# Kernel optimization log

Hardware: AMD Instinct MI355X
Metric: run time of the kernel (lower is better)

## Reference

```python
import jax, jax.numpy as jnp
import numpy as np

N, R, B, H, C, E = 4096, 8, 30, 64, 16, 131072


def setup_inputs() -> dict:
    key = jax.random.key(0)
    ks = jax.random.split(key, 11)
    s = 0.02  # small init scale for weights
    return {
        "x": jax.random.normal(ks[0], (N, N), jnp.float32),
        "edge_index": jax.random.randint(ks[1], (2, E), 0, N, jnp.int32),
        "edge_type": jax.random.randint(ks[2], (E,), 0, R, jnp.int32),
        "basis1": jax.random.normal(ks[3], (B, N, H), jnp.float32) * s,
        "att1": jax.random.normal(ks[4], (R, B), jnp.float32) * s,
        "root1": jax.random.normal(ks[5], (N, H), jnp.float32) * s,
        "bias1": jnp.zeros((H,), jnp.float32),
        "basis2": jax.random.normal(ks[6], (B, H, C), jnp.float32) * s,
        "att2": jax.random.normal(ks[7], (R, B), jnp.float32) * s,
        "root2": jax.random.normal(ks[8], (H, C), jnp.float32) * s,
        "bias2": jnp.zeros((C,), jnp.float32),
    }


def _rgcn_conv(x, src, dst, etype, deg_inv, basis, att, root, bias):
    # Basis-decomposed relation weights: W_r = sum_b att[r,b] * basis[b]
    W = jnp.einsum("rb,bio->rio", att, basis)            # [R, in, out]
    # Pre-transform every node by every relation weight (equivalent to
    # per-edge bmm(x_j, W[edge_type]) but avoids gathering [E, in] features).
    h = jnp.einsum("ni,rio->nro", x, W)                  # [N, R, out]
    msg = h[src, etype]                                  # [E, out] per-edge message
    agg = jax.ops.segment_sum(msg, dst, num_segments=N)  # scatter-add to dst
    agg = agg * deg_inv[:, None]                         # scatter-mean (aggr='mean')
    return agg + x @ root + bias                         # root/self transform + bias


def reference(x, edge_index, edge_type, basis1, att1, root1, bias1,
              basis2, att2, root2, bias2):
    src, dst = edge_index[0], edge_index[1]
    deg = jax.ops.segment_sum(jnp.ones((E,), jnp.float32), dst, num_segments=N)
    deg_inv = 1.0 / jnp.maximum(deg, 1.0)  # zero in-degree -> 0 output, as scatter_mean
    h = jax.nn.relu(_rgcn_conv(x, src, dst, edge_type, deg_inv,
                               basis1, att1, root1, bias1))
    out = _rgcn_conv(h, src, dst, edge_type, deg_inv,
                     basis2, att2, root2, bias2)
    return jax.nn.log_softmax(out, axis=1)
```

## Files before the change

### kernel.cpp

```cpp
#include <hip/hip_runtime.h>
#include <cstdint>

#define E_CNT 131072
#define N_CNT 4096

typedef short bf16x8 __attribute__((ext_vector_type(8)));
typedef float f32x4 __attribute__((ext_vector_type(4)));

__device__ __forceinline__ ushort f2bf(float f) {
  union { float f; unsigned u; } v; v.f = f;
  unsigned r = v.u + 0x7FFFu + ((v.u >> 16) & 1u);
  return (ushort)(r >> 16);
}

__global__ __launch_bounds__(256) void k_prep(const float4* __restrict__ x,
                                              ushort* __restrict__ xbf,
                                              const int* __restrict__ dstp,
                                              int* __restrict__ deg,
                                              const float* __restrict__ att1,
                                              const float* __restrict__ basis1,
                                              const float* __restrict__ root1,
                                              ushort* __restrict__ wt1,
                                              int* __restrict__ c1i) {
  __shared__ float sT[32 * 33];
  int bid = blockIdx.x, t = threadIdx.x;
  if (bid < 16384) {
    int i = bid * 256 + t;
    float4 v = x[i];
    ushort4 o;
    o.x = f2bf(v.x); o.y = f2bf(v.y); o.z = f2bf(v.z); o.w = f2bf(v.w);
    *(ushort4*)(xbf + (size_t)i * 4) = o;
  } else if (bid < 16896) {
    int e = (bid - 16384) * 256 + t;
    atomicAdd(&deg[dstp[e]], 1);
  } else if (bid < 17152) {
    int bb = bid - 16896;
    int i0 = (bb >> 1) * 32, o0 = (bb & 1) * 32;
    int ol = t & 31, ir = t >> 5;
    float a[8][4] = {};
    for (int b = 0; b < 30; ++b) {
      float w0 = att1[0 * 30 + b], w1 = att1[1 * 30 + b], w2 = att1[2 * 30 + b], w3 = att1[3 * 30 + b];
      float w4 = att1[4 * 30 + b], w5 = att1[5 * 30 + b], w6 = att1[6 * 30 + b], w7 = att1[7 * 30 + b];
#pragma unroll
      for (int k = 0; k < 4; ++k) {
        float v = basis1[(size_t)b * 262144 + (size_t)(i0 + ir + k * 8) * 64 + o0 + ol];
        a[0][k] += w0 * v; a[1][k] += w1 * v; a[2][k] += w2 * v; a[3][k] += w3 * v;
        a[4][k] += w4 * v; a[5][k] += w5 * v; a[6][k] += w6 * v; a[7][k] += w7 * v;
      }
    }
    for (int r = 0; r < 8; ++r) {
#pragma unroll
      for (int k = 0; k < 4; ++k) sT[ol * 33 + ir + k * 8] = a[r][k];
      __syncthreads();
#pragma unroll
      for (int k = 0; k < 4; ++k) {
        int orow = ir + k * 8, icol = ol;
        wt1[(size_t)(r * 64 + o0 + orow) * 4096 + i0 + icol] = f2bf(sT[orow * 33 + icol]);
      }
      __syncthreads();
    }
  } else if (bid < 17168) {
    int bb = bid - 17152;
    int i0 = bb * 256;
    int ol = t & 31, ir = t >> 5;
    for (int s = 0; s < 8; ++s) {
      int ib = i0 + s * 32;
#pragma unroll
      for (int k = 0; k < 4; ++k) {
      }
      for (int oh = 0; oh < 2; ++oh) {
        int o0 = oh * 32;
#pragma unroll
        for (int k = 0; k < 4; ++k)
          sT[ol * 33 + ir + k * 8] = root1[(size_t)(ib + ir + k * 8) * 64 + o0 + ol];
        __syncthreads();
#pragma unroll
        for (int k = 0; k < 4; ++k) {
          int orow = ir + k * 8, icol = ol;
          wt1[(size_t)(512 + o0 + orow) * 4096 + ib + icol] = f2bf(sT[orow * 33 + icol]);
        }
        __syncthreads();
      }
    }
  } else {
    int flat = (bid - 17168) * 256 + t;
    c1i[flat] = 0;
  }
}

__global__ __launch_bounds__(1024) void k_scan(const int* __restrict__ deg,
                                               int* __restrict__ rowptr,
                                               int* __restrict__ cursor,
                                               float* __restrict__ dinv) {
  __shared__ int part[1024];
  int t = threadIdx.x;
  int base = t * 4;
  int d0 = deg[base], d1 = deg[base + 1], d2 = deg[base + 2], d3 = deg[base + 3];
  int s = d0 + d1 + d2 + d3;
  part[t] = s;
  __syncthreads();
  for (int off = 1; off < 1024; off <<= 1) {
    int v = part[t];
    int u = (t >= off) ? part[t - off] : 0;
    __syncthreads();
    part[t] = v + u;
    __syncthreads();
  }
  int incl = part[t];
  int excl = incl - s;
  int p0 = excl, p1 = excl + d0, p2 = p1 + d1, p3 = p2 + d2;
  rowptr[base] = p0; rowptr[base + 1] = p1; rowptr[base + 2] = p2; rowptr[base + 3] = p3;
  cursor[base] = p0; cursor[base + 1] = p1; cursor[base + 2] = p2; cursor[base + 3] = p3;
  dinv[base]     = 1.0f / fmaxf((float)d0, 1.0f);
  dinv[base + 1] = 1.0f / fmaxf((float)d1, 1.0f);
  dinv[base + 2] = 1.0f / fmaxf((float)d2, 1.0f);
  dinv[base + 3] = 1.0f / fmaxf((float)d3, 1.0f);
  if (t == 1023) rowptr[4096] = incl;
}

__global__ __launch_bounds__(256) void k_mid(const int* __restrict__ srcp,
                                             const int* __restrict__ dstp,
                                             const int* __restrict__ et,
                                             int* __restrict__ cursor,
                                             int* __restrict__ spack,
                                             const float* __restrict__ att2,
                                             const float* __restrict__ basis2,
                                             const float* __restrict__ root2,
                                             float* __restrict__ w2e) {
  int bid = blockIdx.x, t = threadIdx.x;
  if (bid < 512) {
    int e = bid * 256 + t;
    int d = dstp[e];
    int pos = atomicAdd(&cursor[d], 1);
    spack[pos] = (srcp[e] << 3) | et[e];
  } else {
    int r = bid - 512;
    for (int q = t; q < 1024; q += 256) {
      float a = 0.f;
      if (r < 8) {
        for (int b = 0; b < 30; ++b) a += att2[r * 30 + b] * basis2[b * 1024 + q];
      } else {
        a = root2[q];
      }
      w2e[r * 1024 + q] = a;
    }
  }
}

__global__ __launch_bounds__(256, 5) void k_gemm1(const ushort* __restrict__ xbf,
                                                  const ushort* __restrict__ wt1,
                                                  float* __restrict__ c1) {
  __shared__ __align__(16) ushort As[128 * 64];
  __shared__ __align__(16) ushort Bs[64 * 64];
  int bid = blockIdx.x;
  int swz = (bid & 7) * 144 + (bid >> 3);
  int kp = swz / 288, t2 = swz % 288;
  int bm = t2 / 9, bn = t2 % 9;
  int m0 = bm * 128, n0 = bn * 64, kbase = kp * 1024;
  int tid = threadIdx.x;
  int lane = tid & 63, wid = tid >> 6;
  int wm = wid >> 1, wn = wid & 1;

  f32x4 acc[4][2] = {};

  for (int tt = 0; tt < 16; ++tt) {
    int k0 = kbase + tt * 64;
#pragma unroll
    for (int it = 0; it < 4; ++it) {
      int flat = it * 256 + tid;
      int row = flat >> 3, gg = flat & 7;
      int gcol = k0 + ((gg ^ (row & 7)) << 3);
      const ushort* g = xbf + (size_t)(m0 + row) * 4096 + gcol;
      ushort* l = &As[(it * 256 + wid * 64) * 8];
      __builtin_amdgcn_global_load_lds((const __attribute__((address_space(1))) void*)g,
                                       (__attribute__((address_space(3))) void*)l, 16, 0, 0);
    }
#pragma unroll
    for (int it = 0; it < 2; ++it) {
      int flat = it * 256 + tid;
      int row = flat >> 3, gg = flat & 7;
      int gcol = k0 + ((gg ^ (row & 7)) << 3);
      const ushort* g = wt1 + (size_t)(n0 + row) * 4096 + gcol;
      ushort* l = &Bs[(it * 256 + wid * 64) * 8];
      __builtin_amdgcn_global_load_lds((const __attribute__((address_space(1))) void*)g,
                                       (__attribute__((address_space(3))) void*)l, 16, 0, 0);
    }
    __syncthreads();
    int q = lane >> 4, sw = lane & 7, r16 = lane & 15;
#pragma unroll
    for (int ks = 0; ks < 2; ++ks) {
      int co = ((ks * 4 + q) ^ sw) << 3;
      bf16x8 b0 = *(const bf16x8*)&Bs[(wn * 32 + 0 * 16 + r16) * 64 + co];
      bf16x8 b1 = *(const bf16x8*)&Bs[(wn * 32 + 1 * 16 + r16) * 64 + co];
      bf16x8 a0 = *(const bf16x8*)&As[(wm * 64 + 0 * 16 + r16) * 64 + co];
      bf16x8 a1 = *(const bf16x8*)&As[(wm * 64 + 1 * 16 + r16) * 64 + co];
      bf16x8 a2 = *(const bf16x8*)&As[(wm * 64 + 2 * 16 + r16) * 64 + co];
      bf16x8 a3 = *(const bf16x8*)&As[(wm * 64 + 3 * 16 + r16) * 64 + co];
      __builtin_amdgcn_s_setprio(1);
      acc[0][0] = __builtin_amdgcn_mfma_f32_16x16x32_bf16(a0, b0, acc[0][0], 0, 0, 0);
      acc[0][1] = __builtin_amdgcn_mfma_f32_16x16x32_bf16(a0, b1, acc[0][1], 0, 0, 0);
      acc[1][0] = __builtin_amdgcn_mfma_f32_16x16x32_bf16(a1, b0, acc[1][0], 0, 0, 0);
      acc[1][1] = __builtin_amdgcn_mfma_f32_16x16x32_bf16(a1, b1, acc[1][1], 0, 0, 0);
      acc[2][0] = __builtin_amdgcn_mfma_f32_16x16x32_bf16(a2, b0, acc[2][0], 0, 0, 0);
      acc[2][1] = __builtin_amdgcn_mfma_f32_16x16x32_bf16(a2, b1, acc[2][1], 0, 0, 0);
      acc[3][0] = __builtin_amdgcn_mfma_f32_16x16x32_bf16(a3, b0, acc[3][0], 0, 0, 0);
      acc[3][1] = __builtin_amdgcn_mfma_f32_16x16x32_bf16(a3, b1, acc[3][1], 0, 0, 0);
      __builtin_amdgcn_s_setprio(0);
    }
    __syncthreads();
  }

  int cf = lane & 15, rf4 = (lane >> 4) * 4;
#pragma unroll
  for (int mi = 0; mi < 4; ++mi)
#pragma unroll
    for (int ni = 0; ni < 2; ++ni) {
      int gcol = n0 + wn * 32 + ni * 16 + cf;
#pragma unroll
      for (int j = 0; j < 4; ++j) {
        int grow = m0 + wm * 64 + mi * 16 + rf4 + j;
        atomicAdd(&c1[(size_t)grow * 576 + gcol], acc[mi][ni][j]);
      }
    }
}

__global__ __launch_bounds__(256) void k_agg1h2(const float* __restrict__ c1,
                                                const int* __restrict__ rowptr,
                                                const int* __restrict__ spack,
                                                const float* __restrict__ dinv,
                                                const float* __restrict__ bias1,
                                                const float* __restrict__ w2e,
                                                float* __restrict__ h2c) {
  __shared__ float sh[4][64];
  int g = threadIdx.x >> 6, t = threadIdx.x & 63;
  int n = blockIdx.x * 4 + g;
  int s0 = rowptr[n], s1 = rowptr[n + 1];
  float acc = 0.f;
  int e = s0;
  for (; e + 3 < s1; e += 4) {
    int p0 = spack[e], p1 = spack[e + 1], p2 = spack[e + 2], p3 = spack[e + 3];
    float v0 = c1[(size_t)(p0 >> 3) * 576 + (p0 & 7) * 64 + t];
    float v1 = c1[(size_t)(p1 >> 3) * 576 + (p1 & 7) * 64 + t];
    float v2 = c1[(size_t)(p2 >> 3) * 576 + (p2 & 7) * 64 + t];
    float v3 = c1[(size_t)(p3 >> 3) * 576 + (p3 & 7) * 64 + t];
    acc += (v0 + v1) + (v2 + v3);
  }
  for (; e < s1; ++e) {
    int p = spack[e];
    acc += c1[(size_t)(p >> 3) * 576 + (p & 7) * 64 + t];
  }
  float v = acc * dinv[n] + c1[(size_t)n * 576 + 512 + t] + bias1[t];
  sh[g][t] = fmaxf(v, 0.f);
  __syncthreads();
  float* o = h2c + (size_t)n * 144;
  for (int rc = t; rc < 144; rc += 64) {
    int r9 = rc >> 4, c = rc & 15;
    const float* w = w2e + r9 * 1024 + c;
    float a = 0.f;
#pragma unroll
    for (int hh = 0; hh < 64; ++hh) a += sh[g][hh] * w[hh * 16];
    o[rc] = a;
  }
}

__global__ __launch_bounds__(64) void k_agg2(const float* __restrict__ h2c,
                                             const int* __restrict__ rowptr,
                                             const int* __restrict__ spack,
                                             const float* __restrict__ dinv,
                                             const float* __restrict__ bias2,
                                             float* __restrict__ out) {
  __shared__ float red[64];
  int n = blockIdx.x, t = threadIdx.x;
  int c = t & 15, q = t >> 4;
  int s0 = rowptr[n], s1 = rowptr[n + 1];
  float acc = 0.f;
  for (int e = s0 + q; e < s1; e += 4) {
    int p = spack[e];
    acc += h2c[(size_t)(p >> 3) * 144 + (p & 7) * 16 + c];
  }
  red[t] = acc;
  __syncthreads();
  if (t < 16) {
    float sum = red[c] + red[16 + c] + red[32 + c] + red[48 + c];
    float v = sum * dinv[n] + h2c[(size_t)n * 144 + 128 + c] + bias2[c];
    float m = v;
#pragma unroll
    for (int off = 1; off < 16; off <<= 1) m = fmaxf(m, __shfl_xor(m, off, 64));
    float ex = expf(v - m);
    float s = ex;
#pragma unroll
    for (int off = 1; off < 16; off <<= 1) s += __shfl_xor(s, off, 64);
    out[n * 16 + c] = v - m - logf(s);
  }
}

extern "C" void kernel_launch(void* const* d_in, const int* in_sizes, int n_in,
                              void* d_out, int out_size, void* d_ws, size_t ws_size,
                              hipStream_t stream) {
  const float* x      = (const float*)d_in[0];
  const int*   ei     = (const int*)d_in[1];
  const int*   et     = (const int*)d_in[2];
  const float* basis1 = (const float*)d_in[3];
  const float* att1   = (const float*)d_in[4];
  const float* root1  = (const float*)d_in[5];
  const float* bias1  = (const float*)d_in[6];
  const float* basis2 = (const float*)d_in[7];
  const float* att2   = (const float*)d_in[8];
  const float* root2  = (const float*)d_in[9];
  const float* bias2  = (const float*)d_in[10];
  float* out = (float*)d_out;

  char* ws = (char*)d_ws;
  size_t off = 0;
  auto alloc = [&](size_t bytes) {
    void* p = ws + off;
    off = (off + bytes + 255) & ~(size_t)255;
    return p;
  };
  ushort* xbf  = (ushort*)alloc((size_t)N_CNT * N_CNT * 2);
  ushort* wt1  = (ushort*)alloc((size_t)576 * 4096 * 2);
  float*  c1   = (float*)alloc((size_t)N_CNT * 576 * 4);
  float*  w2e  = (float*)alloc((size_t)9 * 64 * 16 * 4);
  float*  h2c  = (float*)alloc((size_t)N_CNT * 144 * 4);
  int*    deg    = (int*)alloc(4096 * 4);
  float*  dinv   = (float*)alloc(4096 * 4);
  int*    rowptr = (int*)alloc(4097 * 4);
  int*    cursor = (int*)alloc(4096 * 4);
  int*    spack  = (int*)alloc((size_t)E_CNT * 4);

  const int* srcp = ei;
  const int* dstp = ei + E_CNT;

  hipMemsetAsync(deg, 0, 4096 * 4, stream);
  k_prep<<<26384, 256, 0, stream>>>((const float4*)x, xbf, dstp, deg,
                                    att1, basis1, root1, wt1, (int*)c1);
  k_scan<<<1, 1024, 0, stream>>>(deg, rowptr, cursor, dinv);
  k_mid<<<521, 256, 0, stream>>>(srcp, dstp, et, cursor, spack,
                                 att2, basis2, root2, w2e);
  k_gemm1<<<1152, 256, 0, stream>>>(xbf, wt1, c1);
  k_agg1h2<<<1024, 256, 0, stream>>>(c1, rowptr, spack, dinv, bias1, w2e, h2c);
  k_agg2<<<4096, 64, 0, stream>>>(h2c, rowptr, spack, dinv, bias2, out);
}
```

Baseline: 131.4 us.

## Enlarge GEMM1 tile to 256x64 and widen prep kernel per-thread work

The first-layer GEMM block tile grows from 128x64 to 256x64, with each wave computing a 64x64 sub-tile (4x4 MFMA fragments) and the grid halved. This reuses each B fragment across more A rows and cuts redundant B loads and block count, at the cost of more registers and LDS and lower occupancy (launch bounds drop to 3 waves/SIMD-ish). The prep kernel is also reordered so the weight-building blocks launch first, and x conversion and c1 zeroing use wider 16-byte per-thread stores with fewer blocks.

```diff
diff --git a/kernel.cpp b/kernel.cpp
--- a/kernel.cpp
+++ b/kernel.cpp
@@ -21,20 +21,11 @@
                                               const float* __restrict__ basis1,
                                               const float* __restrict__ root1,
                                               ushort* __restrict__ wt1,
-                                              int* __restrict__ c1i) {
+                                              int4* __restrict__ c1v) {
   __shared__ float sT[32 * 33];
   int bid = blockIdx.x, t = threadIdx.x;
-  if (bid < 16384) {
-    int i = bid * 256 + t;
-    float4 v = x[i];
-    ushort4 o;
-    o.x = f2bf(v.x); o.y = f2bf(v.y); o.z = f2bf(v.z); o.w = f2bf(v.w);
-    *(ushort4*)(xbf + (size_t)i * 4) = o;
-  } else if (bid < 16896) {
-    int e = (bid - 16384) * 256 + t;
-    atomicAdd(&deg[dstp[e]], 1);
-  } else if (bid < 17152) {
-    int bb = bid - 16896;
+  if (bid < 256) {
+    int bb = bid;
     int i0 = (bb >> 1) * 32, o0 = (bb & 1) * 32;
     int ol = t & 31, ir = t >> 5;
     float a[8][4] = {};
@@ -59,15 +50,12 @@
       }
       __syncthreads();
     }
-  } else if (bid < 17168) {
-    int bb = bid - 17152;
+  } else if (bid < 272) {
+    int bb = bid - 256;
     int i0 = bb * 256;
     int ol = t & 31, ir = t >> 5;
     for (int s = 0; s < 8; ++s) {
       int ib = i0 + s * 32;
-#pragma unroll
-      for (int k = 0; k < 4; ++k) {
-      }
       for (int oh = 0; oh < 2; ++oh) {
         int o0 = oh * 32;
 #pragma unroll
@@ -82,9 +70,21 @@
         __syncthreads();
       }
     }
+  } else if (bid < 784) {
+    int e = (bid - 272) * 256 + t;
+    atomicAdd(&deg[dstp[e]], 1);
+  } else if (bid < 8976) {
+    int i = (bid - 784) * 256 + t;
+    float4 v0 = x[i * 2], v1 = x[i * 2 + 1];
+    ushort o[8];
+    o[0] = f2bf(v0.x); o[1] = f2bf(v0.y); o[2] = f2bf(v0.z); o[3] = f2bf(v0.w);
+    o[4] = f2bf(v1.x); o[5] = f2bf(v1.y); o[6] = f2bf(v1.z); o[7] = f2bf(v1.w);
+    *(ulonglong2*)(xbf + (size_t)i * 8) = *(const ulonglong2*)o;
   } else {
-    int flat = (bid - 17168) * 256 + t;
-    c1i[flat] = 0;
+    int bb = bid - 8976;
+    int4 z = {0, 0, 0, 0};
+#pragma unroll
+    for (int j = 0; j < 4; ++j) c1v[(size_t)bb * 1024 + j * 256 + t] = z;
   }
 }
 
@@ -147,26 +147,25 @@
   }
 }
 
-__global__ __launch_bounds__(256, 5) void k_gemm1(const ushort* __restrict__ xbf,
+__global__ __launch_bounds__(256, 3) void k_gemm1(const ushort* __restrict__ xbf,
                                                   const ushort* __restrict__ wt1,
                                                   float* __restrict__ c1) {
-  __shared__ __align__(16) ushort As[128 * 64];
+  __shared__ __align__(16) ushort As[256 * 64];
   __shared__ __align__(16) ushort Bs[64 * 64];
   int bid = blockIdx.x;
-  int swz = (bid & 7) * 144 + (bid >> 3);
-  int kp = swz / 288, t2 = swz % 288;
-  int bm = t2 / 9, bn = t2 % 9;
-  int m0 = bm * 128, n0 = bn * 64, kbase = kp * 1024;
+  int swz = (bid & 7) * 72 + (bid >> 3);
+  int kp = swz / 144, rem = swz % 144;
+  int bm = rem / 9, bn = rem % 9;
+  int m0 = bm * 256, n0 = bn * 64, kbase = kp * 1024;
   int tid = threadIdx.x;
   int lane = tid & 63, wid = tid >> 6;
-  int wm = wid >> 1, wn = wid & 1;
-
-  f32x4 acc[4][2] = {};
+
+  f32x4 acc[4][4] = {};
 
   for (int tt = 0; tt < 16; ++tt) {
     int k0 = kbase + tt * 64;
 #pragma unroll
-    for (int it = 0; it < 4; ++it) {
+    for (int it = 0; it < 8; ++it) {
       int flat = it * 256 + tid;
       int row = flat >> 3, gg = flat & 7;
       int gcol = k0 + ((gg ^ (row & 7)) << 3);
@@ -190,21 +189,31 @@
 #pragma unroll
     for (int ks = 0; ks < 2; ++ks) {
       int co = ((ks * 4 + q) ^ sw) << 3;
-      bf16x8 b0 = *(const bf16x8*)&Bs[(wn * 32 + 0 * 16 + r16) * 64 + co];
-      bf16x8 b1 = *(const bf16x8*)&Bs[(wn * 32 + 1 * 16 + r16) * 64 + co];
-      bf16x8 a0 = *(const bf16x8*)&As[(wm * 64 + 0 * 16 + r16) * 64 + co];
-      bf16x8 a1 = *(const bf16x8*)&As[(wm * 64 + 1 * 16 + r16) * 64 + co];
-      bf16x8 a2 = *(const bf16x8*)&As[(wm * 64 + 2 * 16 + r16) * 64 + co];
-      bf16x8 a3 = *(const bf16x8*)&As[(wm * 64 + 3 * 16 + r16) * 64 + co];
+      bf16x8 b0 = *(const bf16x8*)&Bs[(0 * 16 + r16) * 64 + co];
+      bf16x8 b1 = *(const bf16x8*)&Bs[(1 * 16 + r16) * 64 + co];
+      bf16x8 b2 = *(const bf16x8*)&Bs[(2 * 16 + r16) * 64 + co];
+      bf16x8 b3 = *(const bf16x8*)&Bs[(3 * 16 + r16) * 64 + co];
+      bf16x8 a0 = *(const bf16x8*)&As[(wid * 64 + 0 * 16 + r16) * 64 + co];
+      bf16x8 a1 = *(const bf16x8*)&As[(wid * 64 + 1 * 16 + r16) * 64 + co];
+      bf16x8 a2 = *(const bf16x8*)&As[(wid * 64 + 2 * 16 + r16) * 64 + co];
+      bf16x8 a3 = *(const bf16x8*)&As[(wid * 64 + 3 * 16 + r16) * 64 + co];
       __builtin_amdgcn_s_setprio(1);
       acc[0][0] = __builtin_amdgcn_mfma_f32_16x16x32_bf16(a0, b0, acc[0][0], 0, 0, 0);
       acc[0][1] = __builtin_amdgcn_mfma_f32_16x16x32_bf16(a0, b1, acc[0][1], 0, 0, 0);
+      acc[0][2] = __builtin_amdgcn_mfma_f32_16x16x32_bf16(a0, b2, acc[0][2], 0, 0, 0);
+      acc[0][3] = __builtin_amdgcn_mfma_f32_16x16x32_bf16(a0, b3, acc[0][3], 0, 0, 0);
       acc[1][0] = __builtin_amdgcn_mfma_f32_16x16x32_bf16(a1, b0, acc[1][0], 0, 0, 0);
       acc[1][1] = __builtin_amdgcn_mfma_f32_16x16x32_bf16(a1, b1, acc[1][1], 0, 0, 0);
+      acc[1][2] = __builtin_amdgcn_mfma_f32_16x16x32_bf16(a1, b2, acc[1][2], 0, 0, 0);
+      acc[1][3] = __builtin_amdgcn_mfma_f32_16x16x32_bf16(a1, b3, acc[1][3], 0, 0, 0);
       acc[2][0] = __builtin_amdgcn_mfma_f32_16x16x32_bf16(a2, b0, acc[2][0], 0, 0, 0);
       acc[2][1] = __builtin_amdgcn_mfma_f32_16x16x32_bf16(a2, b1, acc[2][1], 0, 0, 0);
+      acc[2][2] = __builtin_amdgcn_mfma_f32_16x16x32_bf16(a2, b2, acc[2][2], 0, 0, 0);
+      acc[2][3] = __builtin_amdgcn_mfma_f32_16x16x32_bf16(a2, b3, acc[2][3], 0, 0, 0);
       acc[3][0] = __builtin_amdgcn_mfma_f32_16x16x32_bf16(a3, b0, acc[3][0], 0, 0, 0);
       acc[3][1] = __builtin_amdgcn_mfma_f32_16x16x32_bf16(a3, b1, acc[3][1], 0, 0, 0);
+      acc[3][2] = __builtin_amdgcn_mfma_f32_16x16x32_bf16(a3, b2, acc[3][2], 0, 0, 0);
+      acc[3][3] = __builtin_amdgcn_mfma_f32_16x16x32_bf16(a3, b3, acc[3][3], 0, 0, 0);
       __builtin_amdgcn_s_setprio(0);
     }
     __syncthreads();
@@ -214,11 +223,11 @@
 #pragma unroll
   for (int mi = 0; mi < 4; ++mi)
 #pragma unroll
-    for (int ni = 0; ni < 2; ++ni) {
-      int gcol = n0 + wn * 32 + ni * 16 + cf;
+    for (int ni = 0; ni < 4; ++ni) {
+      int gcol = n0 + ni * 16 + cf;
 #pragma unroll
       for (int j = 0; j < 4; ++j) {
-        int grow = m0 + wm * 64 + mi * 16 + rf4 + j;
+        int grow = m0 + wid * 64 + mi * 16 + rf4 + j;
         atomicAdd(&c1[(size_t)grow * 576 + gcol], acc[mi][ni][j]);
       }
     }
@@ -332,12 +341,12 @@
   const int* dstp = ei + E_CNT;
 
   hipMemsetAsync(deg, 0, 4096 * 4, stream);
-  k_prep<<<26384, 256, 0, stream>>>((const float4*)x, xbf, dstp, deg,
-                                    att1, basis1, root1, wt1, (int*)c1);
+  k_prep<<<9552, 256, 0, stream>>>((const float4*)x, xbf, dstp, deg,
+                                   att1, basis1, root1, wt1, (int4*)c1);
   k_scan<<<1, 1024, 0, stream>>>(deg, rowptr, cursor, dinv);
   k_mid<<<521, 256, 0, stream>>>(srcp, dstp, et, cursor, spack,
                                  att2, basis2, root2, w2e);
-  k_gemm1<<<1152, 256, 0, stream>>>(xbf, wt1, c1);
+  k_gemm1<<<576, 256, 0, stream>>>(xbf, wt1, c1);
   k_agg1h2<<<1024, 256, 0, stream>>>(c1, rowptr, spack, dinv, bias1, w2e, h2c);
   k_agg2<<<4096, 64, 0, stream>>>(h2c, rowptr, spack, dinv, bias2, out);
 }
```

Result: no change. 131.9 us (+0.4%).

## Replace split-K atomic accumulation with partial buffers plus bf16 reduce kernel

Applied to the files above, without the earlier changes.

The GEMM now writes each split-K partial to its own fp32 buffer instead of doing atomicAdd into a zero-initialised c1, so the zeroing pass in prep goes away. A new reduce kernel sums the four partials and stores the result as bf16, which halves the bytes the gather-heavy aggregation kernel reads. The prep kernel is reordered so the small weight-transform blocks launch first, the x-to-bf16 conversion handles 8 elements per thread, and the basis combination unrolls two bases per step. GEMM occupancy hint goes from 5 to 6. The cost is an extra kernel launch, 4x partial-buffer write and read traffic, and bf16 rounding of the layer-1 activations.

```diff
diff --git a/kernel.cpp b/kernel.cpp
--- a/kernel.cpp
+++ b/kernel.cpp
@@ -11,6 +11,10 @@
   union { float f; unsigned u; } v; v.f = f;
   unsigned r = v.u + 0x7FFFu + ((v.u >> 16) & 1u);
   return (ushort)(r >> 16);
+}
+__device__ __forceinline__ float bf2f(ushort u) {
+  union { unsigned u; float f; } v; v.u = ((unsigned)u) << 16;
+  return v.f;
 }
 
 __global__ __launch_bounds__(256) void k_prep(const float4* __restrict__ x,
@@ -20,32 +24,26 @@
                                               const float* __restrict__ att1,
                                               const float* __restrict__ basis1,
                                               const float* __restrict__ root1,
-                                              ushort* __restrict__ wt1,
-                                              int* __restrict__ c1i) {
+                                              ushort* __restrict__ wt1) {
   __shared__ float sT[32 * 33];
   int bid = blockIdx.x, t = threadIdx.x;
-  if (bid < 16384) {
-    int i = bid * 256 + t;
-    float4 v = x[i];
-    ushort4 o;
-    o.x = f2bf(v.x); o.y = f2bf(v.y); o.z = f2bf(v.z); o.w = f2bf(v.w);
-    *(ushort4*)(xbf + (size_t)i * 4) = o;
-  } else if (bid < 16896) {
-    int e = (bid - 16384) * 256 + t;
-    atomicAdd(&deg[dstp[e]], 1);
-  } else if (bid < 17152) {
-    int bb = bid - 16896;
-    int i0 = (bb >> 1) * 32, o0 = (bb & 1) * 32;
+  if (bid < 256) {
+    int i0 = (bid >> 1) * 32, o0 = (bid & 1) * 32;
     int ol = t & 31, ir = t >> 5;
     float a[8][4] = {};
-    for (int b = 0; b < 30; ++b) {
-      float w0 = att1[0 * 30 + b], w1 = att1[1 * 30 + b], w2 = att1[2 * 30 + b], w3 = att1[3 * 30 + b];
-      float w4 = att1[4 * 30 + b], w5 = att1[5 * 30 + b], w6 = att1[6 * 30 + b], w7 = att1[7 * 30 + b];
+    for (int b = 0; b < 30; b += 2) {
+      float v0[4], v1[4];
 #pragma unroll
       for (int k = 0; k < 4; ++k) {
-        float v = basis1[(size_t)b * 262144 + (size_t)(i0 + ir + k * 8) * 64 + o0 + ol];
-        a[0][k] += w0 * v; a[1][k] += w1 * v; a[2][k] += w2 * v; a[3][k] += w3 * v;
-        a[4][k] += w4 * v; a[5][k] += w5 * v; a[6][k] += w6 * v; a[7][k] += w7 * v;
+        size_t ofs = (size_t)(i0 + ir + k * 8) * 64 + o0 + ol;
+        v0[k] = basis1[(size_t)b * 262144 + ofs];
+        v1[k] = basis1[(size_t)(b + 1) * 262144 + ofs];
+      }
+#pragma unroll
+      for (int r = 0; r < 8; ++r) {
+        float w0 = att1[r * 30 + b], w1 = att1[r * 30 + b + 1];
+#pragma unroll
+        for (int k = 0; k < 4; ++k) a[r][k] += w0 * v0[k] + w1 * v1[k];
       }
     }
     for (int r = 0; r < 8; ++r) {
@@ -59,32 +57,33 @@
       }
       __syncthreads();
     }
-  } else if (bid < 17168) {
-    int bb = bid - 17152;
-    int i0 = bb * 256;
+  } else if (bid < 384) {
+    int bb = bid - 256;
+    int i0 = bb * 32;
     int ol = t & 31, ir = t >> 5;
-    for (int s = 0; s < 8; ++s) {
-      int ib = i0 + s * 32;
+    for (int oh = 0; oh < 2; ++oh) {
+      int o0 = oh * 32;
+#pragma unroll
+      for (int k = 0; k < 4; ++k)
+        sT[ol * 33 + ir + k * 8] = root1[(size_t)(i0 + ir + k * 8) * 64 + o0 + ol];
+      __syncthreads();
 #pragma unroll
       for (int k = 0; k < 4; ++k) {
-      }
-      for (int oh = 0; oh < 2; ++oh) {
-        int o0 = oh * 32;
-#pragma unroll
-        for (int k = 0; k < 4; ++k)
-          sT[ol * 33 + ir + k * 8] = root1[(size_t)(ib + ir + k * 8) * 64 + o0 + ol];
-        __syncthreads();
-#pragma unroll
-        for (int k = 0; k < 4; ++k) {
-          int orow = ir + k * 8, icol = ol;
-          wt1[(size_t)(512 + o0 + orow) * 4096 + ib + icol] = f2bf(sT[orow * 33 + icol]);
-        }
-        __syncthreads();
-      }
-    }
+        int orow = ir + k * 8, icol = ol;
+        wt1[(size_t)(512 + o0 + orow) * 4096 + i0 + icol] = f2bf(sT[orow * 33 + icol]);
+      }
+      __syncthreads();
+    }
+  } else if (bid < 896) {
+    int e = (bid - 384) * 256 + t;
+    atomicAdd(&deg[dstp[e]], 1);
   } else {
-    int flat = (bid - 17168) * 256 + t;
-    c1i[flat] = 0;
+    int i = (bid - 896) * 256 + t;
+    float4 v0 = x[i * 2], v1 = x[i * 2 + 1];
+    ushort o[8];
+    o[0] = f2bf(v0.x); o[1] = f2bf(v0.y); o[2] = f2bf(v0.z); o[3] = f2bf(v0.w);
+    o[4] = f2bf(v1.x); o[5] = f2bf(v1.y); o[6] = f2bf(v1.z); o[7] = f2bf(v1.w);
+    *(ulonglong2*)(xbf + (size_t)i * 8) = *(const ulonglong2*)o;
   }
 }
 
@@ -147,15 +146,15 @@
   }
 }
 
-__global__ __launch_bounds__(256, 5) void k_gemm1(const ushort* __restrict__ xbf,
+__global__ __launch_bounds__(256, 6) void k_gemm1(const ushort* __restrict__ xbf,
                                                   const ushort* __restrict__ wt1,
-                                                  float* __restrict__ c1) {
+                                                  float* __restrict__ c1p) {
   __shared__ __align__(16) ushort As[128 * 64];
   __shared__ __align__(16) ushort Bs[64 * 64];
   int bid = blockIdx.x;
   int swz = (bid & 7) * 144 + (bid >> 3);
-  int kp = swz / 288, t2 = swz % 288;
-  int bm = t2 / 9, bn = t2 % 9;
+  int kp = swz / 288, rem = swz % 288;
+  int bm = rem / 9, bn = rem % 9;
   int m0 = bm * 128, n0 = bn * 64, kbase = kp * 1024;
   int tid = threadIdx.x;
   int lane = tid & 63, wid = tid >> 6;
@@ -210,6 +209,7 @@
     __syncthreads();
   }
 
+  float* outp = c1p + (size_t)kp * 2359296;
   int cf = lane & 15, rf4 = (lane >> 4) * 4;
 #pragma unroll
   for (int mi = 0; mi < 4; ++mi)
@@ -219,12 +219,32 @@
 #pragma unroll
       for (int j = 0; j < 4; ++j) {
         int grow = m0 + wm * 64 + mi * 16 + rf4 + j;
-        atomicAdd(&c1[(size_t)grow * 576 + gcol], acc[mi][ni][j]);
-      }
-    }
-}
-
-__global__ __launch_bounds__(256) void k_agg1h2(const float* __restrict__ c1,
+        outp[(size_t)grow * 576 + gcol] = acc[mi][ni][j];
+      }
+    }
+}
+
+__global__ __launch_bounds__(256) void k_reduce(const float4* __restrict__ p,
+                                                ushort* __restrict__ c1bf) {
+#pragma unroll
+  for (int j = 0; j < 2; ++j) {
+    int idx = blockIdx.x * 512 + j * 256 + threadIdx.x;
+    float4 a = p[idx];
+    float4 b = p[idx + 589824];
+    float4 c = p[idx + 2 * 589824];
+    float4 d = p[idx + 3 * 589824];
+    float4 s;
+    s.x = (a.x + b.x) + (c.x + d.x);
+    s.y = (a.y + b.y) + (c.y + d.y);
+    s.z = (a.z + b.z) + (c.z + d.z);
+    s.w = (a.w + b.w) + (c.w + d.w);
+    ushort4 o;
+    o.x = f2bf(s.x); o.y = f2bf(s.y); o.z = f2bf(s.z); o.w = f2bf(s.w);
+    *(ushort4*)(c1bf + (size_t)idx * 4) = o;
+  }
+}
+
+__global__ __launch_bounds__(256) void k_agg1h2(const ushort* __restrict__ c1bf,
                                                 const int* __restrict__ rowptr,
                                                 const int* __restrict__ spack,
                                                 const float* __restrict__ dinv,
@@ -239,17 +259,17 @@
   int e = s0;
   for (; e + 3 < s1; e += 4) {
     int p0 = spack[e], p1 = spack[e + 1], p2 = spack[e + 2], p3 = spack[e + 3];
-    float v0 = c1[(size_t)(p0 >> 3) * 576 + (p0 & 7) * 64 + t];
-    float v1 = c1[(size_t)(p1 >> 3) * 576 + (p1 & 7) * 64 + t];
-    float v2 = c1[(size_t)(p2 >> 3) * 576 + (p2 & 7) * 64 + t];
-    float v3 = c1[(size_t)(p3 >> 3) * 576 + (p3 & 7) * 64 + t];
+    float v0 = bf2f(c1bf[(size_t)(p0 >> 3) * 576 + (p0 & 7) * 64 + t]);
+    float v1 = bf2f(c1bf[(size_t)(p1 >> 3) * 576 + (p1 & 7) * 64 + t]);
+    float v2 = bf2f(c1bf[(size_t)(p2 >> 3) * 576 + (p2 & 7) * 64 + t]);
+    float v3 = bf2f(c1bf[(size_t)(p3 >> 3) * 576 + (p3 & 7) * 64 + t]);
     acc += (v0 + v1) + (v2 + v3);
   }
   for (; e < s1; ++e) {
     int p = spack[e];
-    acc += c1[(size_t)(p >> 3) * 576 + (p & 7) * 64 + t];
-  }
-  float v = acc * dinv[n] + c1[(size_t)n * 576 + 512 + t] + bias1[t];
+    acc += bf2f(c1bf[(size_t)(p >> 3) * 576 + (p & 7) * 64 + t]);
+  }
+  float v = acc * dinv[n] + bf2f(c1bf[(size_t)n * 576 + 512 + t]) + bias1[t];
   sh[g][t] = fmaxf(v, 0.f);
   __syncthreads();
   float* o = h2c + (size_t)n * 144;
@@ -319,7 +339,8 @@
   };
   ushort* xbf  = (ushort*)alloc((size_t)N_CNT * N_CNT * 2);
   ushort* wt1  = (ushort*)alloc((size_t)576 * 4096 * 2);
-  float*  c1   = (float*)alloc((size_t)N_CNT * 576 * 4);
+  float*  c1p  = (float*)alloc((size_t)4 * N_CNT * 576 * 4);
+  ushort* c1bf = (ushort*)alloc((size_t)N_CNT * 576 * 2);
   float*  w2e  = (float*)alloc((size_t)9 * 64 * 16 * 4);
   float*  h2c  = (float*)alloc((size_t)N_CNT * 144 * 4);
   int*    deg    = (int*)alloc(4096 * 4);
@@ -332,12 +353,13 @@
   const int* dstp = ei + E_CNT;
 
   hipMemsetAsync(deg, 0, 4096 * 4, stream);
-  k_prep<<<26384, 256, 0, stream>>>((const float4*)x, xbf, dstp, deg,
-                                    att1, basis1, root1, wt1, (int*)c1);
+  k_prep<<<9088, 256, 0, stream>>>((const float4*)x, xbf, dstp, deg,
+                                   att1, basis1, root1, wt1);
   k_scan<<<1, 1024, 0, stream>>>(deg, rowptr, cursor, dinv);
   k_mid<<<521, 256, 0, stream>>>(srcp, dstp, et, cursor, spack,
                                  att2, basis2, root2, w2e);
-  k_gemm1<<<1152, 256, 0, stream>>>(xbf, wt1, c1);
-  k_agg1h2<<<1024, 256, 0, stream>>>(c1, rowptr, spack, dinv, bias1, w2e, h2c);
+  k_gemm1<<<1152, 256, 0, stream>>>(xbf, wt1, c1p);
+  k_reduce<<<1152, 256, 0, stream>>>((const float4*)c1p, c1bf);
+  k_agg1h2<<<1024, 256, 0, stream>>>(c1bf, rowptr, spack, dinv, bias1, w2e, h2c);
   k_agg2<<<4096, 64, 0, stream>>>(h2c, rowptr, spack, dinv, bias2, out);
 }
```

Result: slower. 134.5 us (+2.3%).

## Fuse fp32-to-bf16 conversion of x into GEMM tile loads

Applied to the files above, without the earlier changes.

Removes the separate pass that converts the 4096x4096 x matrix to bf16 in the prep kernel. The GEMM now loads fp32 x directly into registers, converts to bf16 and stores into LDS, which drops a 64MB read plus 32MB write/read round trip. The cost is twice the global bytes per A tile inside the GEMM and a loss of the async global-to-LDS path for A. It also remaps block swizzling so each XCD handles one K-split and half of the M range, moves the c1 zeroing to a memset, and restructures the basis combine loop.

```diff
diff --git a/kernel.cpp b/kernel.cpp
--- a/kernel.cpp
+++ b/kernel.cpp
@@ -13,39 +13,31 @@
   return (ushort)(r >> 16);
 }
 
-__global__ __launch_bounds__(256) void k_prep(const float4* __restrict__ x,
-                                              ushort* __restrict__ xbf,
-                                              const int* __restrict__ dstp,
-                                              int* __restrict__ deg,
-                                              const float* __restrict__ att1,
-                                              const float* __restrict__ basis1,
-                                              const float* __restrict__ root1,
-                                              ushort* __restrict__ wt1,
-                                              int* __restrict__ c1i) {
+__global__ __launch_bounds__(256) void k_combine(const float* __restrict__ att1,
+                                                 const float* __restrict__ basis1,
+                                                 const float* __restrict__ root1,
+                                                 ushort* __restrict__ wt1,
+                                                 const int* __restrict__ dstp,
+                                                 int* __restrict__ deg) {
   __shared__ float sT[32 * 33];
   int bid = blockIdx.x, t = threadIdx.x;
-  if (bid < 16384) {
-    int i = bid * 256 + t;
-    float4 v = x[i];
-    ushort4 o;
-    o.x = f2bf(v.x); o.y = f2bf(v.y); o.z = f2bf(v.z); o.w = f2bf(v.w);
-    *(ushort4*)(xbf + (size_t)i * 4) = o;
-  } else if (bid < 16896) {
-    int e = (bid - 16384) * 256 + t;
-    atomicAdd(&deg[dstp[e]], 1);
-  } else if (bid < 17152) {
-    int bb = bid - 16896;
-    int i0 = (bb >> 1) * 32, o0 = (bb & 1) * 32;
+  if (bid < 256) {
+    int i0 = (bid >> 1) * 32, o0 = (bid & 1) * 32;
     int ol = t & 31, ir = t >> 5;
     float a[8][4] = {};
-    for (int b = 0; b < 30; ++b) {
-      float w0 = att1[0 * 30 + b], w1 = att1[1 * 30 + b], w2 = att1[2 * 30 + b], w3 = att1[3 * 30 + b];
-      float w4 = att1[4 * 30 + b], w5 = att1[5 * 30 + b], w6 = att1[6 * 30 + b], w7 = att1[7 * 30 + b];
+    for (int b = 0; b < 30; b += 2) {
+      float v0[4], v1[4];
 #pragma unroll
       for (int k = 0; k < 4; ++k) {
-        float v = basis1[(size_t)b * 262144 + (size_t)(i0 + ir + k * 8) * 64 + o0 + ol];
-        a[0][k] += w0 * v; a[1][k] += w1 * v; a[2][k] += w2 * v; a[3][k] += w3 * v;
-        a[4][k] += w4 * v; a[5][k] += w5 * v; a[6][k] += w6 * v; a[7][k] += w7 * v;
+        size_t ofs = (size_t)(i0 + ir + k * 8) * 64 + o0 + ol;
+        v0[k] = basis1[(size_t)b * 262144 + ofs];
+        v1[k] = basis1[(size_t)(b + 1) * 262144 + ofs];
+      }
+#pragma unroll
+      for (int r = 0; r < 8; ++r) {
+        float w0 = att1[r * 30 + b], w1 = att1[r * 30 + b + 1];
+#pragma unroll
+        for (int k = 0; k < 4; ++k) a[r][k] += w0 * v0[k] + w1 * v1[k];
       }
     }
     for (int r = 0; r < 8; ++r) {
@@ -59,32 +51,26 @@
       }
       __syncthreads();
     }
-  } else if (bid < 17168) {
-    int bb = bid - 17152;
-    int i0 = bb * 256;
+  } else if (bid < 384) {
+    int bb = bid - 256;
+    int i0 = bb * 32;
     int ol = t & 31, ir = t >> 5;
-    for (int s = 0; s < 8; ++s) {
-      int ib = i0 + s * 32;
+    for (int oh = 0; oh < 2; ++oh) {
+      int o0 = oh * 32;
+#pragma unroll
+      for (int k = 0; k < 4; ++k)
+        sT[ol * 33 + ir + k * 8] = root1[(size_t)(i0 + ir + k * 8) * 64 + o0 + ol];
+      __syncthreads();
 #pragma unroll
       for (int k = 0; k < 4; ++k) {
-      }
-      for (int oh = 0; oh < 2; ++oh) {
-        int o0 = oh * 32;
-#pragma unroll
-        for (int k = 0; k < 4; ++k)
-          sT[ol * 33 + ir + k * 8] = root1[(size_t)(ib + ir + k * 8) * 64 + o0 + ol];
-        __syncthreads();
-#pragma unroll
-        for (int k = 0; k < 4; ++k) {
-          int orow = ir + k * 8, icol = ol;
-          wt1[(size_t)(512 + o0 + orow) * 4096 + ib + icol] = f2bf(sT[orow * 33 + icol]);
-        }
-        __syncthreads();
-      }
+        int orow = ir + k * 8, icol = ol;
+        wt1[(size_t)(512 + o0 + orow) * 4096 + i0 + icol] = f2bf(sT[orow * 33 + icol]);
+      }
+      __syncthreads();
     }
   } else {
-    int flat = (bid - 17168) * 256 + t;
-    c1i[flat] = 0;
+    int e = (bid - 384) * 256 + t;
+    atomicAdd(&deg[dstp[e]], 1);
   }
 }
 
@@ -147,15 +133,15 @@
   }
 }
 
-__global__ __launch_bounds__(256, 5) void k_gemm1(const ushort* __restrict__ xbf,
+__global__ __launch_bounds__(256, 5) void k_gemm1(const float* __restrict__ x,
                                                   const ushort* __restrict__ wt1,
                                                   float* __restrict__ c1) {
   __shared__ __align__(16) ushort As[128 * 64];
   __shared__ __align__(16) ushort Bs[64 * 64];
   int bid = blockIdx.x;
-  int swz = (bid & 7) * 144 + (bid >> 3);
-  int kp = swz / 288, t2 = swz % 288;
-  int bm = t2 / 9, bn = t2 % 9;
+  int xcd = bid & 7, idx = bid >> 3;
+  int bn = idx % 9, mk = idx / 9;
+  int kp = xcd >> 1, bm = ((xcd & 1) << 4) + mk;
   int m0 = bm * 128, n0 = bn * 64, kbase = kp * 1024;
   int tid = threadIdx.x;
   int lane = tid & 63, wid = tid >> 6;
@@ -165,15 +151,14 @@
 
   for (int tt = 0; tt < 16; ++tt) {
     int k0 = kbase + tt * 64;
+    float4 va[4][2];
 #pragma unroll
     for (int it = 0; it < 4; ++it) {
       int flat = it * 256 + tid;
       int row = flat >> 3, gg = flat & 7;
-      int gcol = k0 + ((gg ^ (row & 7)) << 3);
-      const ushort* g = xbf + (size_t)(m0 + row) * 4096 + gcol;
-      ushort* l = &As[(it * 256 + wid * 64) * 8];
-      __builtin_amdgcn_global_load_lds((const __attribute__((address_space(1))) void*)g,
-                                       (__attribute__((address_space(3))) void*)l, 16, 0, 0);
+      const float* src = x + (size_t)(m0 + row) * 4096 + k0 + ((gg ^ (row & 7)) << 3);
+      va[it][0] = *(const float4*)src;
+      va[it][1] = *(const float4*)(src + 4);
     }
 #pragma unroll
     for (int it = 0; it < 2; ++it) {
@@ -184,6 +169,14 @@
       ushort* l = &Bs[(it * 256 + wid * 64) * 8];
       __builtin_amdgcn_global_load_lds((const __attribute__((address_space(1))) void*)g,
                                        (__attribute__((address_space(3))) void*)l, 16, 0, 0);
+    }
+#pragma unroll
+    for (int it = 0; it < 4; ++it) {
+      int flat = it * 256 + tid;
+      float4 v0 = va[it][0], v1 = va[it][1];
+      ushort o8[8] = {f2bf(v0.x), f2bf(v0.y), f2bf(v0.z), f2bf(v0.w),
+                      f2bf(v1.x), f2bf(v1.y), f2bf(v1.z), f2bf(v1.w)};
+      *(ulonglong2*)&As[flat * 8] = *(const ulonglong2*)o8;
     }
     __syncthreads();
     int q = lane >> 4, sw = lane & 7, r16 = lane & 15;
@@ -317,7 +310,6 @@
     off = (off + bytes + 255) & ~(size_t)255;
     return p;
   };
-  ushort* xbf  = (ushort*)alloc((size_t)N_CNT * N_CNT * 2);
   ushort* wt1  = (ushort*)alloc((size_t)576 * 4096 * 2);
   float*  c1   = (float*)alloc((size_t)N_CNT * 576 * 4);
   float*  w2e  = (float*)alloc((size_t)9 * 64 * 16 * 4);
@@ -332,12 +324,12 @@
   const int* dstp = ei + E_CNT;
 
   hipMemsetAsync(deg, 0, 4096 * 4, stream);
-  k_prep<<<26384, 256, 0, stream>>>((const float4*)x, xbf, dstp, deg,
-                                    att1, basis1, root1, wt1, (int*)c1);
+  hipMemsetAsync(c1, 0, (size_t)N_CNT * 576 * 4, stream);
+  k_combine<<<896, 256, 0, stream>>>(att1, basis1, root1, wt1, dstp, deg);
   k_scan<<<1, 1024, 0, stream>>>(deg, rowptr, cursor, dinv);
   k_mid<<<521, 256, 0, stream>>>(srcp, dstp, et, cursor, spack,
                                  att2, basis2, root2, w2e);
-  k_gemm1<<<1152, 256, 0, stream>>>(xbf, wt1, c1);
+  k_gemm1<<<1152, 256, 0, stream>>>(x, wt1, c1);
   k_agg1h2<<<1024, 256, 0, stream>>>(c1, rowptr, spack, dinv, bias1, w2e, h2c);
   k_agg2<<<4096, 64, 0, stream>>>(h2c, rowptr, spack, dinv, bias2, out);
 }
```

New measurement: 139.7 us. +6.3%, slower.
